# Performance work log

Hardware: AMD Instinct MI355X
Metric: run time of the kernel (lower is better)

Reference implementation:

```python
import jax, jax.numpy as jnp
import numpy as np

MAX_DISP = 4  # displacement radius -> 9x9 = 81 shifts


def setup_inputs() -> dict:
    key = jax.random.key(0)
    k1, k2 = jax.random.split(key)
    B, C, H, W = 8, 256, 96, 160
    tensorFirst = jax.random.normal(k1, (B, C, H, W), dtype=jnp.float32)
    tensorSecond = jax.random.normal(k2, (B, C, H, W), dtype=jnp.float32)
    return {"tensorFirst": tensorFirst, "tensorSecond": tensorSecond}


def reference(tensorFirst, tensorSecond):
    # Multi-displacement cross-correlation cost volume (FlowNet/PWC-Net style).
    # For each of the 81 displacements (dy, dx) in [-4, 4]^2:
    #   out[b, i*9+j, y, x] = mean_c( input1[b,c,y,x] * input2[b,c,y+dy,x+dx] )
    # (zero-padded outside the image), matching the torch fallback exactly
    # (sum over channels / channels == mean over channels).
    B, C, H, W = tensorFirst.shape
    p2 = jnp.pad(
        tensorSecond,
        ((0, 0), (0, 0), (MAX_DISP, MAX_DISP), (MAX_DISP, MAX_DISP)),
    )
    outs = []
    for dy in range(-MAX_DISP, MAX_DISP + 1):  # fixed 9-step loop (static shifts)
        for dx in range(-MAX_DISP, MAX_DISP + 1):
            shifted = p2[:, :, MAX_DISP + dy:MAX_DISP + dy + H,
                         MAX_DISP + dx:MAX_DISP + dx + W]
            outs.append(jnp.mean(tensorFirst * shifted, axis=1))  # [B, H, W]
    return jnp.stack(outs, axis=1)  # [B, 81, H, W]
```

## Files before the change

### kernel.cpp

```cpp
#include <hip/hip_runtime.h>
#include <hip/hip_fp16.h>

#define CH 256
#define HH 96
#define WW 160
#define HW (HH * WW)

typedef _Float16 half8 __attribute__((ext_vector_type(8)));
typedef float f32x4 __attribute__((ext_vector_type(4)));

__device__ inline unsigned pk2f(float a, float b) {
    return (unsigned)__half_as_ushort(__float2half(a)) |
           ((unsigned)__half_as_ushort(__float2half(b)) << 16);
}

__global__ __launch_bounds__(256, 3)
void corr_v4(const float* __restrict__ Fp, const float* __restrict__ Sp,
             float* __restrict__ out) {
    __shared__ uint4 sS[12 * 128];

    const int bid = blockIdx.x;
    const int b   = bid & 7;
    const int rem = bid >> 3;
    const int y0  = (rem / 10) * 4;
    const int x0  = (rem % 10) * 16;

    const int t    = threadIdx.x;
    const int lane = t & 63;
    const int wv   = t >> 6;
    const int q    = lane >> 4;
    const int n    = lane & 15;

    const float* Fb = Fp + (size_t)b * CH * HW;
    const float* Sb = Sp + (size_t)b * CH * HW;

    const int np = lane & 7;
    const int qq = (lane >> 3) & 3;
    const int jt = (lane >> 5) & 1;
    const int gx = x0 - 4 + jt * 16 + np * 2;
    const bool xok = (gx >= 0) & (gx + 1 < WW);

    bool okv[3];
    const float2* pS[3];
#pragma unroll
    for (int i = 0; i < 3; i++) {
        const int row = i * 4 + wv;
        const int gy  = y0 - 4 + row;
        okv[i] = ((unsigned)gy < HH) & xok;
        const size_t off = okv[i] ? ((size_t)(qq * 8) * HW +
                                     (size_t)gy * WW + gx) : 0;
        pS[i] = (const float2*)(Sb + off);
    }
    const float* pF = Fb + (size_t)(q * 8) * HW + (y0 + wv) * WW + x0 + n;

    float2 rawS[3][8];
    float  rawF[8];

    auto load_raw = [&]() {
#pragma unroll
        for (int i = 0; i < 3; i++)
#pragma unroll
            for (int j = 0; j < 8; j++)
                rawS[i][j] = pS[i][(size_t)j * (HW / 2)];
#pragma unroll
        for (int j = 0; j < 8; j++)
            rawF[j] = pF[(size_t)j * HW];
#pragma unroll
        for (int i = 0; i < 3; i++) pS[i] += (size_t)16 * HW;
        pF += (size_t)32 * HW;
    };

    f32x4 acc[9][2];
#pragma unroll
    for (int dy = 0; dy < 9; dy++) {
        f32x4 z = {0.f, 0.f, 0.f, 0.f};
        acc[dy][0] = z;
        acc[dy][1] = z;
    }

    load_raw();

#pragma unroll 1
    for (int ch = 0; ch < 8; ch++) {
        __syncthreads();

        half8 av;
#pragma unroll
        for (int j = 0; j < 8; j++) av[j] = (_Float16)rawF[j];
#pragma unroll
        for (int i = 0; i < 3; i++) {
            float2 ld[8];
#pragma unroll
            for (int j = 0; j < 8; j++) {
                ld[j].x = okv[i] ? rawS[i][j].x : 0.0f;
                ld[j].y = okv[i] ? rawS[i][j].y : 0.0f;
            }
            uint4 v0, v1;
            v0.x = pk2f(ld[0].x, ld[1].x);
            v0.y = pk2f(ld[2].x, ld[3].x);
            v0.z = pk2f(ld[4].x, ld[5].x);
            v0.w = pk2f(ld[6].x, ld[7].x);
            v1.x = pk2f(ld[0].y, ld[1].y);
            v1.y = pk2f(ld[2].y, ld[3].y);
            v1.z = pk2f(ld[4].y, ld[5].y);
            v1.w = pk2f(ld[6].y, ld[7].y);
            uint4* dst = &sS[(i * 4 + wv) * 128 + lane * 2];
            dst[0] = v0;
            dst[1] = v1;
        }
        __syncthreads();

        if (ch < 7) load_raw();

#pragma unroll
        for (int dy = 0; dy < 9; dy++) {
            const int row = wv + dy;
            half8 b0 = *(const half8*)(sS + row * 128 + lane);
            half8 b1 = *(const half8*)(sS + row * 128 + 64 + lane);
            acc[dy][0] = __builtin_amdgcn_mfma_f32_16x16x32_f16(av, b0, acc[dy][0], 0, 0, 0);
            acc[dy][1] = __builtin_amdgcn_mfma_f32_16x16x32_f16(av, b1, acc[dy][1], 0, 0, 0);
        }
    }

    const int y = y0 + wv;
#pragma unroll
    for (int r = 0; r < 4; r++) {
        const int m = q * 4 + r;
#pragma unroll
        for (int jtt = 0; jtt < 2; jtt++) {
            const int dxp = jtt * 16 + n - m;
            if (dxp >= 0 && dxp <= 8) {
                float* p = out + ((size_t)(b * 81 + dxp) * HH + y) * WW + x0 + m;
#pragma unroll
                for (int dy = 0; dy < 9; dy++) {
                    p[(size_t)dy * 9 * HW] = acc[dy][jtt][r] * (1.0f / 256.0f);
                }
            }
        }
    }
}

extern "C" void kernel_launch(void* const* d_in, const int* in_sizes, int n_in,
                              void* d_out, int out_size, void* d_ws, size_t ws_size,
                              hipStream_t stream) {
    const float* F = (const float*)d_in[0];
    const float* S = (const float*)d_in[1];
    float* o = (float*)d_out;
    corr_v4<<<dim3(1920), dim3(256), 0, stream>>>(F, S, o);
}
```

Measured before the change: 325.1 us.

## Double-buffer shared tiles, use 16x16x16 MFMA, and raise occupancy target

Processes channels in 16 chunks of 16 instead of 8 chunks of 32, using the smaller 16x16x16 f16 MFMA with 4-element operands. Shared memory is double-buffered, so each iteration needs one barrier instead of two and the next chunk can be committed while the current one is consumed. Register demand for the raw staging arrays is halved, and launch bounds now request 4 blocks per CU. The trade-off is twice as many loop iterations and barriers, plus the lower per-instruction throughput of the smaller MFMA shape.

New measurement: 328.6 us. Within noise of the previous version (+1.1%).

```diff
diff --git a/kernel.cpp b/kernel.cpp
--- a/kernel.cpp
+++ b/kernel.cpp
@@ -6,7 +6,7 @@
 #define WW 160
 #define HW (HH * WW)
 
-typedef _Float16 half8 __attribute__((ext_vector_type(8)));
+typedef _Float16 h4 __attribute__((ext_vector_type(4)));
 typedef float f32x4 __attribute__((ext_vector_type(4)));
 
 __device__ inline unsigned pk2f(float a, float b) {
@@ -14,10 +14,10 @@
            ((unsigned)__half_as_ushort(__float2half(b)) << 16);
 }
 
-__global__ __launch_bounds__(256, 3)
-void corr_v4(const float* __restrict__ Fp, const float* __restrict__ Sp,
+__global__ __launch_bounds__(256, 4)
+void corr_v5(const float* __restrict__ Fp, const float* __restrict__ Sp,
              float* __restrict__ out) {
-    __shared__ uint4 sS[12 * 128];
+    __shared__ uint2 sS[2 * 12 * 128];
 
     const int bid = blockIdx.x;
     const int b   = bid & 7;
@@ -31,8 +31,8 @@
     const int q    = lane >> 4;
     const int n    = lane & 15;
 
-    const float* Fb = Fp + (size_t)b * CH * HW;
-    const float* Sb = Sp + (size_t)b * CH * HW;
+    const float*  Fb  = Fp + (size_t)b * CH * HW;
+    const float2* Sb2 = (const float2*)(Sp + (size_t)b * CH * HW);
 
     const int np = lane & 7;
     const int qq = (lane >> 3) & 3;
@@ -41,33 +41,56 @@
     const bool xok = (gx >= 0) & (gx + 1 < WW);
 
     bool okv[3];
-    const float2* pS[3];
+    int  sOff[3];
 #pragma unroll
     for (int i = 0; i < 3; i++) {
         const int row = i * 4 + wv;
         const int gy  = y0 - 4 + row;
         okv[i] = ((unsigned)gy < HH) & xok;
-        const size_t off = okv[i] ? ((size_t)(qq * 8) * HW +
-                                     (size_t)gy * WW + gx) : 0;
-        pS[i] = (const float2*)(Sb + off);
+        sOff[i] = okv[i] ? (qq * 4) * (HW / 2) + gy * (WW / 2) + (gx >> 1) : 0;
     }
-    const float* pF = Fb + (size_t)(q * 8) * HW + (y0 + wv) * WW + x0 + n;
+    int fOff = (q * 4) * HW + (y0 + wv) * WW + x0 + n;
 
-    float2 rawS[3][8];
-    float  rawF[8];
+    float2 rawS[3][4];
+    float  rawF[4];
+    h4     av;
 
     auto load_raw = [&]() {
 #pragma unroll
         for (int i = 0; i < 3; i++)
 #pragma unroll
-            for (int j = 0; j < 8; j++)
-                rawS[i][j] = pS[i][(size_t)j * (HW / 2)];
+            for (int j = 0; j < 4; j++)
+                rawS[i][j] = Sb2[sOff[i] + j * (HW / 2)];
 #pragma unroll
-        for (int j = 0; j < 8; j++)
-            rawF[j] = pF[(size_t)j * HW];
+        for (int j = 0; j < 4; j++)
+            rawF[j] = Fb[fOff + j * HW];
 #pragma unroll
-        for (int i = 0; i < 3; i++) pS[i] += (size_t)16 * HW;
-        pF += (size_t)32 * HW;
+        for (int i = 0; i < 3; i++) sOff[i] += 8 * HW;
+        fOff += 16 * HW;
+    };
+
+    const int wrow = jt * 64 + qq * 16 + np * 2;
+
+    auto commit = [&](int wb) {
+        h4 a;
+#pragma unroll
+        for (int j = 0; j < 4; j++) a[j] = (_Float16)rawF[j];
+        av = a;
+#pragma unroll
+        for (int i = 0; i < 3; i++) {
+            float ax[4], ay[4];
+#pragma unroll
+            for (int j = 0; j < 4; j++) {
+                ax[j] = okv[i] ? rawS[i][j].x : 0.0f;
+                ay[j] = okv[i] ? rawS[i][j].y : 0.0f;
+            }
+            uint4 v;
+            v.x = pk2f(ax[0], ax[1]);
+            v.y = pk2f(ax[2], ax[3]);
+            v.z = pk2f(ay[0], ay[1]);
+            v.w = pk2f(ay[2], ay[3]);
+            *(uint4*)&sS[wb + (i * 4 + wv) * 128 + wrow] = v;
+        }
     };
 
     f32x4 acc[9][2];
@@ -79,46 +102,27 @@
     }
 
     load_raw();
+    commit(0);
+    load_raw();
+    __syncthreads();
 
 #pragma unroll 1
-    for (int ch = 0; ch < 8; ch++) {
-        __syncthreads();
-
-        half8 av;
-#pragma unroll
-        for (int j = 0; j < 8; j++) av[j] = (_Float16)rawF[j];
-#pragma unroll
-        for (int i = 0; i < 3; i++) {
-            float2 ld[8];
-#pragma unroll
-            for (int j = 0; j < 8; j++) {
-                ld[j].x = okv[i] ? rawS[i][j].x : 0.0f;
-                ld[j].y = okv[i] ? rawS[i][j].y : 0.0f;
-            }
-            uint4 v0, v1;
-            v0.x = pk2f(ld[0].x, ld[1].x);
-            v0.y = pk2f(ld[2].x, ld[3].x);
-            v0.z = pk2f(ld[4].x, ld[5].x);
-            v0.w = pk2f(ld[6].x, ld[7].x);
-            v1.x = pk2f(ld[0].y, ld[1].y);
-            v1.y = pk2f(ld[2].y, ld[3].y);
-            v1.z = pk2f(ld[4].y, ld[5].y);
-            v1.w = pk2f(ld[6].y, ld[7].y);
-            uint4* dst = &sS[(i * 4 + wv) * 128 + lane * 2];
-            dst[0] = v0;
-            dst[1] = v1;
-        }
-        __syncthreads();
-
-        if (ch < 7) load_raw();
+    for (int ch = 0; ch < 16; ch++) {
+        const int rb = (ch & 1) ? 1536 : 0;
+        const uint2* rp = sS + rb + wv * 128 + q * 16 + n;
 
 #pragma unroll
         for (int dy = 0; dy < 9; dy++) {
-            const int row = wv + dy;
-            half8 b0 = *(const half8*)(sS + row * 128 + lane);
-            half8 b1 = *(const half8*)(sS + row * 128 + 64 + lane);
-            acc[dy][0] = __builtin_amdgcn_mfma_f32_16x16x32_f16(av, b0, acc[dy][0], 0, 0, 0);
-            acc[dy][1] = __builtin_amdgcn_mfma_f32_16x16x32_f16(av, b1, acc[dy][1], 0, 0, 0);
+            h4 b0 = *(const h4*)(rp + dy * 128);
+            h4 b1 = *(const h4*)(rp + dy * 128 + 64);
+            acc[dy][0] = __builtin_amdgcn_mfma_f32_16x16x16f16(av, b0, acc[dy][0], 0, 0, 0);
+            acc[dy][1] = __builtin_amdgcn_mfma_f32_16x16x16f16(av, b1, acc[dy][1], 0, 0, 0);
+        }
+
+        if (ch < 15) {
+            commit(1536 - rb);
+            if (ch < 14) load_raw();
+            __syncthreads();
         }
     }
 
@@ -146,5 +150,5 @@
     const float* F = (const float*)d_in[0];
     const float* S = (const float*)d_in[1];
     float* o = (float*)d_out;
-    corr_v4<<<dim3(1920), dim3(256), 0, stream>>>(F, S, o);
+    corr_v5<<<dim3(1920), dim3(256), 0, stream>>>(F, S, o);
 }
```
